# Kernel tuning notes

Hardware: AMD Instinct MI355X
Metric: run time of the kernel (lower is better)

The kernel has to match this reference:

```python
import jax, jax.numpy as jnp
import numpy as np

N = 50000      # nodes per graph batch (per siamese side)
E = 500000     # edges per side
F_IN = 128     # input_channels
H = 128        # hidden_channels
OUT = 2        # output_channels
G = 512        # number of graphs in the batch


def setup_inputs() -> dict:
    key = jax.random.key(0)
    ks = jax.random.split(key, 16)

    def lin_w(k, fan_in, shape):
        lim = 1.0 / np.sqrt(fan_in)
        return jax.random.uniform(k, shape, jnp.float32, -lim, lim)

    return {
        "x1": jax.random.normal(ks[0], (N, F_IN), jnp.float32),
        "x2": jax.random.normal(ks[1], (N, F_IN), jnp.float32),
        "edge_index1": jax.random.randint(ks[2], (2, E), 0, N, jnp.int32),
        "edge_index2": jax.random.randint(ks[3], (2, E), 0, N, jnp.int32),
        "batch1": jnp.sort(jax.random.randint(ks[4], (N,), 0, G, jnp.int32)),
        "batch2": jnp.sort(jax.random.randint(ks[5], (N,), 0, G, jnp.int32)),
        "W1": lin_w(ks[6], F_IN, (F_IN, H)), "b1": jnp.zeros((H,), jnp.float32),
        "W2": lin_w(ks[7], H, (H, H)),       "b2": jnp.zeros((H,), jnp.float32),
        "W3": lin_w(ks[8], H, (H, H)),       "b3": jnp.zeros((H,), jnp.float32),
        "Wc1": lin_w(ks[9], 2 * H, (2 * H, 4 * H)), "bc1": jnp.zeros((4 * H,), jnp.float32),
        "Wc2": lin_w(ks[10], 4 * H, (4 * H, 2 * H)), "bc2": jnp.zeros((2 * H,), jnp.float32),
        "Wc3": lin_w(ks[11], 2 * H, (2 * H, OUT)),   "bc3": jnp.zeros((OUT,), jnp.float32),
        "num_graphs": G,
    }


def _gcn_layer(x, W, b, src, dst, dinv):
    # PyG GCNConv: linear transform, then deg^{-1/2} A_hat deg^{-1/2} aggregation + bias
    h = x @ W
    msg = h[src] * (dinv[src] * dinv[dst])[:, None]   # [E+N, H]
    return jax.ops.segment_sum(msg, dst, num_segments=x.shape[0]) + b


def _forward_once(x, edge_index, batch, W1, b1, W2, b2, W3, b3, num_graphs):
    n = x.shape[0]
    loop = jnp.arange(n, dtype=edge_index.dtype)
    src = jnp.concatenate([edge_index[0], loop])      # add self-loops
    dst = jnp.concatenate([edge_index[1], loop])
    deg = jax.ops.segment_sum(jnp.ones_like(dst, dtype=x.dtype), dst, num_segments=n)
    dinv = jax.lax.rsqrt(deg)                          # deg >= 1 due to self-loops
    h = jax.nn.relu(_gcn_layer(x, W1, b1, src, dst, dinv))
    h = jax.nn.relu(_gcn_layer(h, W2, b2, src, dst, dinv))
    h = _gcn_layer(h, W3, b3, src, dst, dinv)
    # global_mean_pool over batch indices
    s = jax.ops.segment_sum(h, batch, num_segments=num_graphs)
    cnt = jax.ops.segment_sum(jnp.ones((n,), x.dtype), batch, num_segments=num_graphs)
    return s / jnp.maximum(cnt, 1.0)[:, None]


def reference(x1, x2, edge_index1, edge_index2, batch1, batch2,
              W1, b1, W2, b2, W3, b3, Wc1, bc1, Wc2, bc2, Wc3, bc3, num_graphs):
    g1 = _forward_once(x1, edge_index1, batch1, W1, b1, W2, b2, W3, b3, num_graphs)
    g2 = _forward_once(x2, edge_index2, batch2, W1, b1, W2, b2, W3, b3, num_graphs)
    z = jnp.concatenate([g1, g2], axis=1)             # [G, 2H]
    z = jax.nn.relu(z @ Wc1 + bc1)
    z = jax.nn.relu(z @ Wc2 + bc2)
    # dropout p=0.5 is identity at eval time
    return z @ Wc3 + bc3                               # [G, OUT]
```

## Files before the change

kernel.cpp:

```cpp
#include <hip/hip_runtime.h>
#include <math.h>

#define N_NODES 50000
#define E_EDGES 500000
#define HDIM    128
#define OUTC    2
#define NGRAPH  512

typedef _Float16 f16x8 __attribute__((ext_vector_type(8)));
typedef float    f32x4 __attribute__((ext_vector_type(4)));

__device__ inline float2 unpack2(unsigned u) {
    union { unsigned v; _Float16 h[2]; } c; c.v = u;
    return make_float2((float)c.h[0], (float)c.h[1]);
}
__device__ inline unsigned pack2(float a, float b) {
    union { _Float16 h[2]; unsigned u; } c;
    c.h[0] = (_Float16)a; c.h[1] = (_Float16)b;
    return c.u;
}

__global__ void k_hist(const int* __restrict__ d0, const int* __restrict__ d1,
                       int ecnt, int off1, int* __restrict__ cnt,
                       const float* __restrict__ W1, const float* __restrict__ W2,
                       _Float16* __restrict__ w1hi, _Float16* __restrict__ w1lo,
                       _Float16* __restrict__ w2hi, _Float16* __restrict__ w2lo) {
    int i = blockIdx.x * blockDim.x + threadIdx.x;
    int stride = gridDim.x * blockDim.x;
    for (int j = i; j < 128 * 128; j += stride) {
        int n = j >> 7, k = j & 127;
        float v = W1[k * 128 + n];
        _Float16 h = (_Float16)v;
        w1hi[j] = h; w1lo[j] = (_Float16)(v - (float)h);
        v = W2[k * 128 + n];
        h = (_Float16)v;
        w2hi[j] = h; w2lo[j] = (_Float16)(v - (float)h);
    }
    for (int j = i; j < ecnt; j += stride) {
        int d = (j < E_EDGES) ? d0[j] : d1[j - E_EDGES] + off1;
        atomicAdd(&cnt[d], 1);
    }
}

__global__ void k_scan_a(const int* __restrict__ cnt, int* __restrict__ excl,
                         int* __restrict__ blksum, float* __restrict__ dinv,
                         const int* __restrict__ bt0, const int* __restrict__ bt1,
                         int goff0, int nn, int nside, float* __restrict__ cnt_g) {
    __shared__ int s[512];
    int t = threadIdx.x;
    int i = blockIdx.x * 512 + t;
    int v = 0;
    if (i < nn) {
        v = cnt[i];
        dinv[i] = 1.0f / sqrtf((float)(v + 1));
        int g = (i < nside) ? bt0[i] + goff0 : bt1[i - nside] + NGRAPH;
        atomicAdd(&cnt_g[g], 1.0f);
    }
    s[t] = v; __syncthreads();
    for (int off = 1; off < 512; off <<= 1) {
        int add = (t >= off) ? s[t - off] : 0;
        __syncthreads();
        s[t] += add;
        __syncthreads();
    }
    if (i < nn) excl[i] = s[t] - v;
    if (t == 511) blksum[blockIdx.x] = s[511];
}

__global__ void k_scan_b(int* __restrict__ blksum, int nb) {
    __shared__ int s[512];
    int t = threadIdx.x;
    int v = (t < nb) ? blksum[t] : 0;
    s[t] = v; __syncthreads();
    for (int off = 1; off < 512; off <<= 1) {
        int add = (t >= off) ? s[t - off] : 0;
        __syncthreads();
        s[t] += add;
        __syncthreads();
    }
    if (t < nb) blksum[t] = s[t] - v;
}

__global__ void k_scan_c(int* __restrict__ excl, const int* __restrict__ blksum,
                         int* __restrict__ cursor, int nn, int tot) {
    int t = threadIdx.x;
    int i = blockIdx.x * 512 + t;
    if (i < nn) {
        int v = excl[i] + blksum[blockIdx.x];
        excl[i] = v;
        cursor[i] = v;
    }
    if (i == 0) excl[nn] = tot;
}

__global__ void k_fill(const int* __restrict__ s0, const int* __restrict__ s1,
                       const int* __restrict__ d0, const int* __restrict__ d1,
                       int ecnt, int off1, int goff0,
                       const int* __restrict__ bt0, const int* __restrict__ bt1,
                       int* __restrict__ cursor,
                       const float* __restrict__ dinv, int2* __restrict__ edges,
                       int* __restrict__ gdst) {
    int i = blockIdx.x * blockDim.x + threadIdx.x;
    int stride = gridDim.x * blockDim.x;
    for (; i < ecnt; i += stride) {
        int d, sg, g;
        if (i < E_EDGES) {
            int dl = d0[i];
            sg = s0[i]; d = dl; g = bt0[dl] + goff0;
        } else {
            int dl = d1[i - E_EDGES];
            sg = s1[i - E_EDGES] + off1; d = dl + off1; g = bt1[dl] + NGRAPH;
        }
        int p = atomicAdd(&cursor[d], 1);
        float w = dinv[sg] * dinv[d];
        edges[p] = make_int2(sg, __float_as_int(w));
        gdst[p] = g;
    }
}

__device__ inline void cvt8(const float4& p, const float4& q, f16x8& h, f16x8& l) {
    float v[8] = {p.x, p.y, p.z, p.w, q.x, q.y, q.z, q.w};
#pragma unroll
    for (int i = 0; i < 8; i++) {
        _Float16 hh = (_Float16)v[i];
        h[i] = hh;
        l[i] = (_Float16)(v[i] - (float)hh);
    }
}

template <int ASRC>
__global__ __launch_bounds__(256) void k_gemm_split(
        const float* __restrict__ A0f, const float* __restrict__ A1f, int nside,
        const _Float16* __restrict__ Ahi, const _Float16* __restrict__ Alo,
        const _Float16* __restrict__ Bhi, const _Float16* __restrict__ Blo,
        _Float16* __restrict__ C, int M) {
    __shared__ _Float16 sA[2][128][40];
    __shared__ _Float16 sB[2][128][40];
    int tid = threadIdx.x;
    int wave = tid >> 6, lane = tid & 63;
    int wm = (wave >> 1) * 64;
    int wn = (wave & 1) * 64;
    int quad = lane >> 4, fm = lane & 15;
    int row0 = blockIdx.x * 128;

    int lr = tid >> 2;
    int lk = (tid & 3) * 8;

    f32x4 acc[4][4] = {};
    const float4 z4 = make_float4(0.f, 0.f, 0.f, 0.f);

    for (int kc = 0; kc < 128; kc += 32) {
        int r1 = row0 + lr, r2 = row0 + lr + 64;
        bool ok1 = r1 < M, ok2 = r2 < M;
        f16x8 ah1, al1, ah2, al2;
        if (ASRC == 1) {
            const float* p1 = (r1 < nside) ? A0f + (size_t)r1 * 128
                                           : A1f + (size_t)(r1 - nside) * 128;
            const float* p2 = (r2 < nside) ? A0f + (size_t)r2 * 128
                                           : A1f + (size_t)(r2 - nside) * 128;
            float4 a = ok1 ? *(const float4*)(p1 + kc + lk) : z4;
            float4 b = ok1 ? *(const float4*)(p1 + kc + lk + 4) : z4;
            float4 c = ok2 ? *(const float4*)(p2 + kc + lk) : z4;
            float4 d = ok2 ? *(const float4*)(p2 + kc + lk + 4) : z4;
            cvt8(a, b, ah1, al1);
            cvt8(c, d, ah2, al2);
        } else {
            const f16x8 zf = {};
            ah1 = ok1 ? *(const f16x8*)(Ahi + (size_t)r1 * 128 + kc + lk) : zf;
            al1 = ok1 ? *(const f16x8*)(Alo + (size_t)r1 * 128 + kc + lk) : zf;
            ah2 = ok2 ? *(const f16x8*)(Ahi + (size_t)r2 * 128 + kc + lk) : zf;
            al2 = ok2 ? *(const f16x8*)(Alo + (size_t)r2 * 128 + kc + lk) : zf;
        }
        f16x8 bh1 = *(const f16x8*)(Bhi + (size_t)lr * 128 + kc + lk);
        f16x8 bl1 = *(const f16x8*)(Blo + (size_t)lr * 128 + kc + lk);
        f16x8 bh2 = *(const f16x8*)(Bhi + (size_t)(lr + 64) * 128 + kc + lk);
        f16x8 bl2 = *(const f16x8*)(Blo + (size_t)(lr + 64) * 128 + kc + lk);
        __syncthreads();
        *(f16x8*)&sA[0][lr][lk]      = ah1;
        *(f16x8*)&sA[1][lr][lk]      = al1;
        *(f16x8*)&sA[0][lr + 64][lk] = ah2;
        *(f16x8*)&sA[1][lr + 64][lk] = al2;
        *(f16x8*)&sB[0][lr][lk]      = bh1;
        *(f16x8*)&sB[1][lr][lk]      = bl1;
        *(f16x8*)&sB[0][lr + 64][lk] = bh2;
        *(f16x8*)&sB[1][lr + 64][lk] = bl2;
        __syncthreads();

        f16x8 afh[4], afl[4], bfh[4], bfl[4];
#pragma unroll
        for (int mi = 0; mi < 4; mi++) {
            afh[mi] = *(const f16x8*)&sA[0][wm + mi * 16 + fm][quad * 8];
            afl[mi] = *(const f16x8*)&sA[1][wm + mi * 16 + fm][quad * 8];
        }
#pragma unroll
        for (int ni = 0; ni < 4; ni++) {
            bfh[ni] = *(const f16x8*)&sB[0][wn + ni * 16 + fm][quad * 8];
            bfl[ni] = *(const f16x8*)&sB[1][wn + ni * 16 + fm][quad * 8];
        }
#pragma unroll
        for (int mi = 0; mi < 4; mi++)
#pragma unroll
            for (int ni = 0; ni < 4; ni++) {
                acc[mi][ni] = __builtin_amdgcn_mfma_f32_16x16x32_f16(afh[mi], bfh[ni], acc[mi][ni], 0, 0, 0);
                acc[mi][ni] = __builtin_amdgcn_mfma_f32_16x16x32_f16(afh[mi], bfl[ni], acc[mi][ni], 0, 0, 0);
                acc[mi][ni] = __builtin_amdgcn_mfma_f32_16x16x32_f16(afl[mi], bfh[ni], acc[mi][ni], 0, 0, 0);
            }
    }

#pragma unroll
    for (int mi = 0; mi < 4; mi++)
#pragma unroll
        for (int reg = 0; reg < 4; reg++) {
            int r = row0 + wm + mi * 16 + quad * 4 + reg;
            if (r >= M) continue;
#pragma unroll
            for (int ni = 0; ni < 4; ni++)
                C[(size_t)r * 128 + wn + ni * 16 + fm] = (_Float16)acc[mi][ni][reg];
        }
}

__global__ __launch_bounds__(256) void k_gemm(
        const float* __restrict__ A, const float* __restrict__ B,
        const float* __restrict__ bias, float* __restrict__ C,
        int M, int Nn, int K, int ldc, int act) {
    __shared__ float As[16][64];
    __shared__ float Bs[16][68];
    int tid = threadIdx.x;
    int tx = tid & 15, ty = tid >> 4;
    int row0 = blockIdx.x * 64, col0 = blockIdx.y * 64;
    float acc[4][4] = {};
    int arow = tid >> 2;
    int acol = (tid & 3) * 4;
    int brow = tid >> 4;
    int bcol = (tid & 15) * 4;

    for (int k0 = 0; k0 < K; k0 += 16) {
        float4 av = make_float4(0.f, 0.f, 0.f, 0.f);
        int ar = row0 + arow;
        if (ar < M) av = *(const float4*)(A + (size_t)ar * K + k0 + acol);
        As[acol + 0][arow] = av.x;
        As[acol + 1][arow] = av.y;
        As[acol + 2][arow] = av.z;
        As[acol + 3][arow] = av.w;

        float4 bv = make_float4(0.f, 0.f, 0.f, 0.f);
        const float* Brow = B + (size_t)(k0 + brow) * Nn;
        int bc = col0 + bcol;
        if (bc + 3 < Nn) {
            bv = *(const float4*)(Brow + bc);
        } else {
            if (bc     < Nn) bv.x = Brow[bc];
            if (bc + 1 < Nn) bv.y = Brow[bc + 1];
            if (bc + 2 < Nn) bv.z = Brow[bc + 2];
        }
        Bs[brow][bcol + 0] = bv.x;
        Bs[brow][bcol + 1] = bv.y;
        Bs[brow][bcol + 2] = bv.z;
        Bs[brow][bcol + 3] = bv.w;
        __syncthreads();

#pragma unroll
        for (int k = 0; k < 16; k++) {
            float4 a = *(const float4*)&As[k][ty * 4];
            float4 b = *(const float4*)&Bs[k][tx * 4];
            acc[0][0] += a.x * b.x; acc[0][1] += a.x * b.y; acc[0][2] += a.x * b.z; acc[0][3] += a.x * b.w;
            acc[1][0] += a.y * b.x; acc[1][1] += a.y * b.y; acc[1][2] += a.y * b.z; acc[1][3] += a.y * b.w;
            acc[2][0] += a.z * b.x; acc[2][1] += a.z * b.y; acc[2][2] += a.z * b.z; acc[2][3] += a.z * b.w;
            acc[3][0] += a.w * b.x; acc[3][1] += a.w * b.y; acc[3][2] += a.w * b.z; acc[3][3] += a.w * b.w;
        }
        __syncthreads();
    }

#pragma unroll
    for (int i = 0; i < 4; i++) {
        int r = row0 + ty * 4 + i;
        if (r >= M) continue;
#pragma unroll
        for (int j = 0; j < 4; j++) {
            int c = col0 + tx * 4 + j;
            if (c >= Nn) continue;
            float v = acc[i][j];
            if (bias) v += bias[c];
            if (act) v = fmaxf(v, 0.0f);
            C[(size_t)r * ldc + c] = v;
        }
    }
}

__global__ __launch_bounds__(256) void k_gemm_pool(
        const float* __restrict__ pool, const float* __restrict__ cnt_g,
        const float* __restrict__ W, const float* __restrict__ bias,
        float* __restrict__ zcat) {
    __shared__ float As[16][64];
    __shared__ float Bs[16][68];
    int side = blockIdx.z;
    const float* A = pool + (size_t)side * NGRAPH * HDIM;
    const float* cg = cnt_g + side * NGRAPH;
    int tid = threadIdx.x;
    int tx = tid & 15, ty = tid >> 4;
    int row0 = blockIdx.x * 64, col0 = blockIdx.y * 64;
    float acc[4][4] = {};
    int arow = tid >> 2;
    int acol = (tid & 3) * 4;
    int brow = tid >> 4;
    int bcol = (tid & 15) * 4;

    for (int k0 = 0; k0 < 128; k0 += 16) {
        int ar = row0 + arow;
        float sc = 1.0f / fmaxf(cg[ar], 1.0f);
        float4 av = *(const float4*)(A + (size_t)ar * 128 + k0 + acol);
        As[acol + 0][arow] = av.x * sc;
        As[acol + 1][arow] = av.y * sc;
        As[acol + 2][arow] = av.z * sc;
        As[acol + 3][arow] = av.w * sc;

        float4 bv = *(const float4*)(W + (size_t)(k0 + brow) * 128 + col0 + bcol);
        Bs[brow][bcol + 0] = bv.x;
        Bs[brow][bcol + 1] = bv.y;
        Bs[brow][bcol + 2] = bv.z;
        Bs[brow][bcol + 3] = bv.w;
        __syncthreads();

#pragma unroll
        for (int k = 0; k < 16; k++) {
            float4 a = *(const float4*)&As[k][ty * 4];
            float4 b = *(const float4*)&Bs[k][tx * 4];
            acc[0][0] += a.x * b.x; acc[0][1] += a.x * b.y; acc[0][2] += a.x * b.z; acc[0][3] += a.x * b.w;
            acc[1][0] += a.y * b.x; acc[1][1] += a.y * b.y; acc[1][2] += a.y * b.z; acc[1][3] += a.y * b.w;
            acc[2][0] += a.z * b.x; acc[2][1] += a.z * b.y; acc[2][2] += a.z * b.z; acc[2][3] += a.z * b.w;
            acc[3][0] += a.w * b.x; acc[3][1] += a.w * b.y; acc[3][2] += a.w * b.z; acc[3][3] += a.w * b.w;
        }
        __syncthreads();
    }

#pragma unroll
    for (int i = 0; i < 4; i++) {
        int r = row0 + ty * 4 + i;
#pragma unroll
        for (int j = 0; j < 4; j++) {
            int c = col0 + tx * 4 + j;
            zcat[(size_t)r * 256 + side * 128 + c] = acc[i][j] + bias[c];
        }
    }
}

template <int PACK>
__global__ __launch_bounds__(256) void k_agg(
        const _Float16* __restrict__ H, const float* __restrict__ dinv,
        const int* __restrict__ row_ptr, const int2* __restrict__ edges,
        const float* __restrict__ bias,
        _Float16* __restrict__ outHi, _Float16* __restrict__ outLo,
        int nnodes) {
    int wave = threadIdx.x >> 6, lane = threadIdx.x & 63;
    int node = blockIdx.x * 4 + wave;
    if (node >= nnodes) return;

    float di = dinv[node];
    float2 hv = unpack2(((const unsigned*)(H + (size_t)node * HDIM))[lane]);
    float wself = di * di;
    float ax = hv.x * wself;
    float ay = hv.y * wself;

    int rs = __builtin_amdgcn_readfirstlane(row_ptr[node]);
    int re = __builtin_amdgcn_readfirstlane(row_ptr[node + 1]);

    for (int base = rs; base < re; base += 8) {
        int nrem = re - base, m = nrem - 1;
        int i1 = 1 < nrem ? 1 : m;
        int i2 = 2 < nrem ? 2 : m;
        int i3 = 3 < nrem ? 3 : m;
        int i4 = 4 < nrem ? 4 : m;
        int i5 = 5 < nrem ? 5 : m;
        int i6 = 6 < nrem ? 6 : m;
        int i7 = 7 < nrem ? 7 : m;
        int2 E0 = edges[base];
        int2 E1 = edges[base + i1];
        int2 E2 = edges[base + i2];
        int2 E3 = edges[base + i3];
        int2 E4 = edges[base + i4];
        int2 E5 = edges[base + i5];
        int2 E6 = edges[base + i6];
        int2 E7 = edges[base + i7];
        unsigned u0 = ((const unsigned*)(H + (size_t)E0.x * HDIM))[lane];
        unsigned u1 = ((const unsigned*)(H + (size_t)E1.x * HDIM))[lane];
        unsigned u2 = ((const unsigned*)(H + (size_t)E2.x * HDIM))[lane];
        unsigned u3 = ((const unsigned*)(H + (size_t)E3.x * HDIM))[lane];
        unsigned u4 = ((const unsigned*)(H + (size_t)E4.x * HDIM))[lane];
        unsigned u5 = ((const unsigned*)(H + (size_t)E5.x * HDIM))[lane];
        unsigned u6 = ((const unsigned*)(H + (size_t)E6.x * HDIM))[lane];
        unsigned u7 = ((const unsigned*)(H + (size_t)E7.x * HDIM))[lane];
        float w0 = __int_as_float(E0.y);
        float w1 = 1 < nrem ? __int_as_float(E1.y) : 0.f;
        float w2 = 2 < nrem ? __int_as_float(E2.y) : 0.f;
        float w3 = 3 < nrem ? __int_as_float(E3.y) : 0.f;
        float w4 = 4 < nrem ? __int_as_float(E4.y) : 0.f;
        float w5 = 5 < nrem ? __int_as_float(E5.y) : 0.f;
        float w6 = 6 < nrem ? __int_as_float(E6.y) : 0.f;
        float w7 = 7 < nrem ? __int_as_float(E7.y) : 0.f;
        float2 v0 = unpack2(u0), v1 = unpack2(u1), v2 = unpack2(u2), v3 = unpack2(u3);
        float2 v4 = unpack2(u4), v5 = unpack2(u5), v6 = unpack2(u6), v7 = unpack2(u7);
        ax = fmaf(v0.x, w0, ax); ay = fmaf(v0.y, w0, ay);
        ax = fmaf(v1.x, w1, ax); ay = fmaf(v1.y, w1, ay);
        ax = fmaf(v2.x, w2, ax); ay = fmaf(v2.y, w2, ay);
        ax = fmaf(v3.x, w3, ax); ay = fmaf(v3.y, w3, ay);
        ax = fmaf(v4.x, w4, ax); ay = fmaf(v4.y, w4, ay);
        ax = fmaf(v5.x, w5, ax); ay = fmaf(v5.y, w5, ay);
        ax = fmaf(v6.x, w6, ax); ay = fmaf(v6.y, w6, ay);
        ax = fmaf(v7.x, w7, ax); ay = fmaf(v7.y, w7, ay);
    }

    float ox = fmaxf(ax + bias[lane * 2],     0.0f);
    float oy = fmaxf(ay + bias[lane * 2 + 1], 0.0f);
    if (PACK) {
        _Float16 hx = (_Float16)ox, hy = (_Float16)oy;
        _Float16 lx = (_Float16)(ox - (float)hx), ly = (_Float16)(oy - (float)hy);
        union { _Float16 h[2]; unsigned u; } ph, pl;
        ph.h[0] = hx; ph.h[1] = hy;
        pl.h[0] = lx; pl.h[1] = ly;
        ((unsigned*)(outHi + (size_t)node * HDIM))[lane] = ph.u;
        ((unsigned*)(outLo + (size_t)node * HDIM))[lane] = pl.u;
    } else {
        ((unsigned*)(outHi + (size_t)node * HDIM))[lane] = pack2(ox, oy);
    }
}

__global__ __launch_bounds__(256) void k_sweep3(
        const _Float16* __restrict__ H, const int2* __restrict__ edges,
        const int* __restrict__ gdst, const float* __restrict__ dinv,
        const int* __restrict__ bt0, const int* __restrict__ bt1,
        int goff0, int nnodes, int nside, int nedges,
        float* __restrict__ pool) {
    int lane = threadIdx.x & 63;
    int wid = blockIdx.x * 4 + (threadIdx.x >> 6);
    int ewaves = (nedges + 63) >> 6;

    if (wid < ewaves) {
        int e0 = wid << 6;
        int e1 = e0 + 64; if (e1 > nedges) e1 = nedges;
        int gfirst = __builtin_amdgcn_readfirstlane(gdst[e0]);
        int glast  = __builtin_amdgcn_readfirstlane(gdst[e1 - 1]);
        float ax = 0.f, ay = 0.f;

        if (gfirst == glast) {
            for (int base = e0; base < e1; base += 8) {
                int nrem = e1 - base, m = nrem - 1;
                int i1 = 1 < nrem ? 1 : m;
                int i2 = 2 < nrem ? 2 : m;
                int i3 = 3 < nrem ? 3 : m;
                int i4 = 4 < nrem ? 4 : m;
                int i5 = 5 < nrem ? 5 : m;
                int i6 = 6 < nrem ? 6 : m;
                int i7 = 7 < nrem ? 7 : m;
                int2 E0 = edges[base];
                int2 E1 = edges[base + i1];
                int2 E2 = edges[base + i2];
                int2 E3 = edges[base + i3];
                int2 E4 = edges[base + i4];
                int2 E5 = edges[base + i5];
                int2 E6 = edges[base + i6];
                int2 E7 = edges[base + i7];
                unsigned u0 = ((const unsigned*)(H + (size_t)E0.x * HDIM))[lane];
                unsigned u1 = ((const unsigned*)(H + (size_t)E1.x * HDIM))[lane];
                unsigned u2 = ((const unsigned*)(H + (size_t)E2.x * HDIM))[lane];
                unsigned u3 = ((const unsigned*)(H + (size_t)E3.x * HDIM))[lane];
                unsigned u4 = ((const unsigned*)(H + (size_t)E4.x * HDIM))[lane];
                unsigned u5 = ((const unsigned*)(H + (size_t)E5.x * HDIM))[lane];
                unsigned u6 = ((const unsigned*)(H + (size_t)E6.x * HDIM))[lane];
                unsigned u7 = ((const unsigned*)(H + (size_t)E7.x * HDIM))[lane];
                float w0 = __int_as_float(E0.y);
                float w1 = 1 < nrem ? __int_as_float(E1.y) : 0.f;
                float w2 = 2 < nrem ? __int_as_float(E2.y) : 0.f;
                float w3 = 3 < nrem ? __int_as_float(E3.y) : 0.f;
                float w4 = 4 < nrem ? __int_as_float(E4.y) : 0.f;
                float w5 = 5 < nrem ? __int_as_float(E5.y) : 0.f;
                float w6 = 6 < nrem ? __int_as_float(E6.y) : 0.f;
                float w7 = 7 < nrem ? __int_as_float(E7.y) : 0.f;
                float2 v0 = unpack2(u0), v1 = unpack2(u1), v2 = unpack2(u2), v3 = unpack2(u3);
                float2 v4 = unpack2(u4), v5 = unpack2(u5), v6 = unpack2(u6), v7 = unpack2(u7);
                ax = fmaf(v0.x, w0, ax); ay = fmaf(v0.y, w0, ay);
                ax = fmaf(v1.x, w1, ax); ay = fmaf(v1.y, w1, ay);
                ax = fmaf(v2.x, w2, ax); ay = fmaf(v2.y, w2, ay);
                ax = fmaf(v3.x, w3, ax); ay = fmaf(v3.y, w3, ay);
                ax = fmaf(v4.x, w4, ax); ay = fmaf(v4.y, w4, ay);
                ax = fmaf(v5.x, w5, ax); ay = fmaf(v5.y, w5, ay);
                ax = fmaf(v6.x, w6, ax); ay = fmaf(v6.y, w6, ay);
                ax = fmaf(v7.x, w7, ax); ay = fmaf(v7.y, w7, ay);
            }
            float* p = pool + (size_t)gfirst * HDIM + lane * 2;
            atomicAdd(p, ax); atomicAdd(p + 1, ay);
        } else {
            int gcur = gfirst;
            for (int e = e0; e < e1; e++) {
                int2 E = edges[e];
                int g = __builtin_amdgcn_readfirstlane(gdst[e]);
                if (g != gcur) {
                    float* p = pool + (size_t)gcur * HDIM + lane * 2;
                    atomicAdd(p, ax); atomicAdd(p + 1, ay);
                    ax = 0.f; ay = 0.f;
                    gcur = g;
                }
                float w = __int_as_float(E.y);
                float2 v = unpack2(((const unsigned*)(H + (size_t)E.x * HDIM))[lane]);
                ax = fmaf(v.x, w, ax);
                ay = fmaf(v.y, w, ay);
            }
            float* p = pool + (size_t)gcur * HDIM + lane * 2;
            atomicAdd(p, ax); atomicAdd(p + 1, ay);
        }
    } else {
        int wid2 = wid - ewaves;
        int n0 = wid2 << 6;
        if (n0 >= nnodes) return;
        int n1 = n0 + 64; if (n1 > nnodes) n1 = nnodes;
        float ax = 0.f, ay = 0.f;
        int gcur = (n0 < nside) ? bt0[n0] + goff0 : bt1[n0 - nside] + NGRAPH;
        gcur = __builtin_amdgcn_readfirstlane(gcur);
        for (int n = n0; n < n1; n++) {
            int g = (n < nside) ? bt0[n] + goff0 : bt1[n - nside] + NGRAPH;
            g = __builtin_amdgcn_readfirstlane(g);
            float dn = dinv[n];
            float w = dn * dn;
            float2 v = unpack2(((const unsigned*)(H + (size_t)n * HDIM))[lane]);
            if (g != gcur) {
                float* p = pool + (size_t)gcur * HDIM + lane * 2;
                atomicAdd(p, ax); atomicAdd(p + 1, ay);
                ax = 0.f; ay = 0.f;
                gcur = g;
            }
            ax = fmaf(v.x, w, ax);
            ay = fmaf(v.y, w, ay);
        }
        float* p = pool + (size_t)gcur * HDIM + lane * 2;
        atomicAdd(p, ax); atomicAdd(p + 1, ay);
    }
}

extern "C" void kernel_launch(void* const* d_in, const int* in_sizes, int n_in,
                              void* d_out, int out_size, void* d_ws, size_t ws_size,
                              hipStream_t stream) {
    (void)in_sizes; (void)n_in; (void)out_size;

    const float* x[2]  = {(const float*)d_in[0], (const float*)d_in[1]};
    const int*   ei[2] = {(const int*)d_in[2], (const int*)d_in[3]};
    const int*   bt[2] = {(const int*)d_in[4], (const int*)d_in[5]};
    const float* W1  = (const float*)d_in[6];  const float* b1  = (const float*)d_in[7];
    const float* W2  = (const float*)d_in[8];  const float* b2  = (const float*)d_in[9];
    const float* W3  = (const float*)d_in[10]; const float* b3  = (const float*)d_in[11];
    const float* Wc1 = (const float*)d_in[12]; const float* bc1 = (const float*)d_in[13];
    const float* Wc2 = (const float*)d_in[14]; const float* bc2 = (const float*)d_in[15];
    const float* Wc3 = (const float*)d_in[16]; const float* bc3 = (const float*)d_in[17];
    float* out = (float*)d_out;

    const bool batched = ws_size >= 120ull * 1000 * 1000;
    const int NN = batched ? 2 * N_NODES : N_NODES;
    const int NE = batched ? 2 * E_EDGES : E_EDGES;

    char* ws = (char*)d_ws;
    size_t off = 0;
    auto carve = [&](size_t bytes) -> char* {
        char* p = ws + off;
        off += (bytes + 255) & ~(size_t)255;
        return p;
    };

    int*   edge_cnt = (int*)  carve((size_t)NN * 4);
    int*   cursor   = (int*)  carve((size_t)NN * 4);
    float* pool_s   = (float*)carve((size_t)2 * NGRAPH * HDIM * 4);
    float* cnt_g    = (float*)carve((size_t)2 * NGRAPH * 4);
    float* dinv     = (float*)carve((size_t)NN * 4);
    int*   row_ptr  = (int*)  carve((size_t)(NN + 1) * 4);
    int2*  edges    = (int2*) carve((size_t)NE * 8);
    int*   gdst     = (int*)  carve((size_t)NE * 4);
    int*   blksum   = (int*)  carve(1024 * 4);
    _Float16* wt    = (_Float16*)carve(4 * 128 * 128 * 2);
    _Float16* hS    = (_Float16*)carve((size_t)NN * HDIM * 4);
    _Float16* hA    = (_Float16*)carve((size_t)NN * HDIM * 2);
    float* zcat     = (float*)carve((size_t)NGRAPH * 2 * HDIM * 4);
    float* z1       = (float*)carve((size_t)NGRAPH * 4 * HDIM * 4);
    float* z2       = (float*)carve((size_t)NGRAPH * 2 * HDIM * 4);

    _Float16* w1hi = wt;
    _Float16* w1lo = wt + 128 * 128;
    _Float16* w2hi = wt + 2 * 128 * 128;
    _Float16* w2lo = wt + 3 * 128 * 128;
    _Float16* hShi = hS;
    _Float16* hSlo = hS + (size_t)NN * HDIM;

    const int gblk = (NN + 127) / 128;
    size_t zero_all = (size_t)((char*)cnt_g + 2 * NGRAPH * 4 - (char*)edge_cnt);
    size_t zero_cnt = (size_t)((char*)pool_s - (char*)edge_cnt);

    if (batched) {
        const int nscan = (2 * N_NODES + 511) / 512;
        const int ablk  = (2 * N_NODES + 3) / 4;
        const int swaves = ((2 * E_EDGES + 63) >> 6) + ((2 * N_NODES + 63) >> 6);
        const int sblk = (swaves + 3) / 4;

        hipMemsetAsync(edge_cnt, 0, zero_all, stream);
        k_hist<<<1024, 256, 0, stream>>>(ei[0] + E_EDGES, ei[1] + E_EDGES,
                                         2 * E_EDGES, N_NODES, edge_cnt,
                                         W1, W2, w1hi, w1lo, w2hi, w2lo);
        k_scan_a<<<nscan, 512, 0, stream>>>(edge_cnt, row_ptr, blksum, dinv,
                                            bt[0], bt[1], 0, 2 * N_NODES, N_NODES, cnt_g);
        k_scan_b<<<1, 512, 0, stream>>>(blksum, nscan);
        k_scan_c<<<nscan, 512, 0, stream>>>(row_ptr, blksum, cursor, 2 * N_NODES, 2 * E_EDGES);
        k_fill<<<1024, 256, 0, stream>>>(ei[0], ei[1], ei[0] + E_EDGES, ei[1] + E_EDGES,
                                         2 * E_EDGES, N_NODES, 0, bt[0], bt[1],
                                         cursor, dinv, edges, gdst);

        k_gemm_split<1><<<gblk, 256, 0, stream>>>(x[0], x[1], N_NODES,
                                                  nullptr, nullptr, w1hi, w1lo, hA, 2 * N_NODES);
        k_agg<1><<<ablk, 256, 0, stream>>>(hA, dinv, row_ptr, edges, b1,
                                           hShi, hSlo, 2 * N_NODES);
        k_gemm_split<0><<<gblk, 256, 0, stream>>>(nullptr, nullptr, 0,
                                                  hShi, hSlo, w2hi, w2lo, hA, 2 * N_NODES);
        k_agg<0><<<ablk, 256, 0, stream>>>(hA, dinv, row_ptr, edges, b2,
                                           hShi, nullptr, 2 * N_NODES);
        k_sweep3<<<sblk, 256, 0, stream>>>(hShi, edges, gdst, dinv, bt[0], bt[1],
                                           0, 2 * N_NODES, N_NODES, 2 * E_EDGES, pool_s);
    } else {
        const int nscan = (N_NODES + 511) / 512;
        const int ablk  = (N_NODES + 3) / 4;
        const int swaves = ((E_EDGES + 63) >> 6) + ((N_NODES + 63) >> 6);
        const int sblk = (swaves + 3) / 4;

        for (int s = 0; s < 2; ++s) {
            const int* esrc = ei[s];
            const int* edst = ei[s] + E_EDGES;
            int goff = s * NGRAPH;

            hipMemsetAsync(edge_cnt, 0, s == 0 ? zero_all : zero_cnt, stream);
            k_hist<<<512, 256, 0, stream>>>(edst, edst, E_EDGES, 0, edge_cnt,
                                            W1, W2, w1hi, w1lo, w2hi, w2lo);
            k_scan_a<<<nscan, 512, 0, stream>>>(edge_cnt, row_ptr, blksum, dinv,
                                                bt[s], bt[s], goff, N_NODES, N_NODES, cnt_g);
            k_scan_b<<<1, 512, 0, stream>>>(blksum, nscan);
            k_scan_c<<<nscan, 512, 0, stream>>>(row_ptr, blksum, cursor, N_NODES, E_EDGES);
            k_fill<<<512, 256, 0, stream>>>(esrc, esrc, edst, edst, E_EDGES, 0, goff,
                                            bt[s], bt[s], cursor, dinv, edges, gdst);

            k_gemm_split<1><<<gblk, 256, 0, stream>>>(x[s], x[s], N_NODES,
                                                      nullptr, nullptr, w1hi, w1lo, hA, N_NODES);
            k_agg<1><<<ablk, 256, 0, stream>>>(hA, dinv, row_ptr, edges, b1,
                                               hShi, hSlo, N_NODES);
            k_gemm_split<0><<<gblk, 256, 0, stream>>>(nullptr, nullptr, 0,
                                                      hShi, hSlo, w2hi, w2lo, hA, N_NODES);
            k_agg<0><<<ablk, 256, 0, stream>>>(hA, dinv, row_ptr, edges, b2,
                                               hShi, nullptr, N_NODES);
            k_sweep3<<<sblk, 256, 0, stream>>>(hShi, edges, gdst, dinv, bt[s], bt[s],
                                               goff, N_NODES, N_NODES, E_EDGES, pool_s);
        }
    }

    k_gemm_pool<<<dim3(NGRAPH / 64, 2, 2), 256, 0, stream>>>(pool_s, cnt_g, W3, b3, zcat);

    k_gemm<<<dim3(NGRAPH / 64, (4 * HDIM) / 64), 256, 0, stream>>>(zcat, Wc1, bc1, z1, NGRAPH, 4 * HDIM, 2 * HDIM, 4 * HDIM, 1);
    k_gemm<<<dim3(NGRAPH / 64, (2 * HDIM) / 64), 256, 0, stream>>>(z1, Wc2, bc2, z2, NGRAPH, 2 * HDIM, 4 * HDIM, 2 * HDIM, 1);
    k_gemm<<<dim3(NGRAPH / 64, 1), 256, 0, stream>>>(z2, Wc3, bc3, out, NGRAPH, OUTC, 2 * HDIM, OUTC, 0);
}
```

Before: 589.2 us.

## Pack graph id into int4 edge records and split aggregation loops into full and tail

Each CSR edge record becomes an int4 holding source, weight and graph id, and the separate gdst array is removed. This saves one scattered store in fill and lets the pooling sweep read the graph id from the record it already loads. The aggregation kernel now runs a clamp-free full-8 loop followed by a separate masked tail, and the sweep's single-graph path is unrolled to 16 gathers per iteration to keep more loads in flight. The cost is that each edge record grows from 8 to 16 bytes with 4 padding bytes, so k_agg and the sweep read more edge-array bytes.

After: 579.4 us. Within noise of the previous version (-1.7%).

```diff
diff --git a/kernel.cpp b/kernel.cpp
--- a/kernel.cpp
+++ b/kernel.cpp
@@ -98,8 +98,7 @@
                        int ecnt, int off1, int goff0,
                        const int* __restrict__ bt0, const int* __restrict__ bt1,
                        int* __restrict__ cursor,
-                       const float* __restrict__ dinv, int2* __restrict__ edges,
-                       int* __restrict__ gdst) {
+                       const float* __restrict__ dinv, int4* __restrict__ edges) {
     int i = blockIdx.x * blockDim.x + threadIdx.x;
     int stride = gridDim.x * blockDim.x;
     for (; i < ecnt; i += stride) {
@@ -113,8 +112,7 @@
         }
         int p = atomicAdd(&cursor[d], 1);
         float w = dinv[sg] * dinv[d];
-        edges[p] = make_int2(sg, __float_as_int(w));
-        gdst[p] = g;
+        edges[p] = make_int4(sg, __float_as_int(w), g, 0);
     }
 }
 
@@ -347,7 +345,7 @@
 template <int PACK>
 __global__ __launch_bounds__(256) void k_agg(
         const _Float16* __restrict__ H, const float* __restrict__ dinv,
-        const int* __restrict__ row_ptr, const int2* __restrict__ edges,
+        const int* __restrict__ row_ptr, const int4* __restrict__ edges,
         const float* __restrict__ bias,
         _Float16* __restrict__ outHi, _Float16* __restrict__ outLo,
         int nnodes) {
@@ -364,23 +362,16 @@
     int rs = __builtin_amdgcn_readfirstlane(row_ptr[node]);
     int re = __builtin_amdgcn_readfirstlane(row_ptr[node + 1]);
 
-    for (int base = rs; base < re; base += 8) {
-        int nrem = re - base, m = nrem - 1;
-        int i1 = 1 < nrem ? 1 : m;
-        int i2 = 2 < nrem ? 2 : m;
-        int i3 = 3 < nrem ? 3 : m;
-        int i4 = 4 < nrem ? 4 : m;
-        int i5 = 5 < nrem ? 5 : m;
-        int i6 = 6 < nrem ? 6 : m;
-        int i7 = 7 < nrem ? 7 : m;
-        int2 E0 = edges[base];
-        int2 E1 = edges[base + i1];
-        int2 E2 = edges[base + i2];
-        int2 E3 = edges[base + i3];
-        int2 E4 = edges[base + i4];
-        int2 E5 = edges[base + i5];
-        int2 E6 = edges[base + i6];
-        int2 E7 = edges[base + i7];
+    int base = rs;
+    for (; base + 8 <= re; base += 8) {
+        int4 E0 = edges[base + 0];
+        int4 E1 = edges[base + 1];
+        int4 E2 = edges[base + 2];
+        int4 E3 = edges[base + 3];
+        int4 E4 = edges[base + 4];
+        int4 E5 = edges[base + 5];
+        int4 E6 = edges[base + 6];
+        int4 E7 = edges[base + 7];
         unsigned u0 = ((const unsigned*)(H + (size_t)E0.x * HDIM))[lane];
         unsigned u1 = ((const unsigned*)(H + (size_t)E1.x * HDIM))[lane];
         unsigned u2 = ((const unsigned*)(H + (size_t)E2.x * HDIM))[lane];
@@ -389,16 +380,12 @@
         unsigned u5 = ((const unsigned*)(H + (size_t)E5.x * HDIM))[lane];
         unsigned u6 = ((const unsigned*)(H + (size_t)E6.x * HDIM))[lane];
         unsigned u7 = ((const unsigned*)(H + (size_t)E7.x * HDIM))[lane];
-        float w0 = __int_as_float(E0.y);
-        float w1 = 1 < nrem ? __int_as_float(E1.y) : 0.f;
-        float w2 = 2 < nrem ? __int_as_float(E2.y) : 0.f;
-        float w3 = 3 < nrem ? __int_as_float(E3.y) : 0.f;
-        float w4 = 4 < nrem ? __int_as_float(E4.y) : 0.f;
-        float w5 = 5 < nrem ? __int_as_float(E5.y) : 0.f;
-        float w6 = 6 < nrem ? __int_as_float(E6.y) : 0.f;
-        float w7 = 7 < nrem ? __int_as_float(E7.y) : 0.f;
         float2 v0 = unpack2(u0), v1 = unpack2(u1), v2 = unpack2(u2), v3 = unpack2(u3);
         float2 v4 = unpack2(u4), v5 = unpack2(u5), v6 = unpack2(u6), v7 = unpack2(u7);
+        float w0 = __int_as_float(E0.y), w1 = __int_as_float(E1.y);
+        float w2 = __int_as_float(E2.y), w3 = __int_as_float(E3.y);
+        float w4 = __int_as_float(E4.y), w5 = __int_as_float(E5.y);
+        float w6 = __int_as_float(E6.y), w7 = __int_as_float(E7.y);
         ax = fmaf(v0.x, w0, ax); ay = fmaf(v0.y, w0, ay);
         ax = fmaf(v1.x, w1, ax); ay = fmaf(v1.y, w1, ay);
         ax = fmaf(v2.x, w2, ax); ay = fmaf(v2.y, w2, ay);
@@ -407,6 +394,39 @@
         ax = fmaf(v5.x, w5, ax); ay = fmaf(v5.y, w5, ay);
         ax = fmaf(v6.x, w6, ax); ay = fmaf(v6.y, w6, ay);
         ax = fmaf(v7.x, w7, ax); ay = fmaf(v7.y, w7, ay);
+    }
+    if (base < re) {
+        int nrem = re - base, m = nrem - 1;
+        int4 E0 = edges[base];
+        int4 E1 = edges[base + (1 < nrem ? 1 : m)];
+        int4 E2 = edges[base + (2 < nrem ? 2 : m)];
+        int4 E3 = edges[base + (3 < nrem ? 3 : m)];
+        int4 E4 = edges[base + (4 < nrem ? 4 : m)];
+        int4 E5 = edges[base + (5 < nrem ? 5 : m)];
+        int4 E6 = edges[base + (6 < nrem ? 6 : m)];
+        unsigned u0 = ((const unsigned*)(H + (size_t)E0.x * HDIM))[lane];
+        unsigned u1 = ((const unsigned*)(H + (size_t)E1.x * HDIM))[lane];
+        unsigned u2 = ((const unsigned*)(H + (size_t)E2.x * HDIM))[lane];
+        unsigned u3 = ((const unsigned*)(H + (size_t)E3.x * HDIM))[lane];
+        unsigned u4 = ((const unsigned*)(H + (size_t)E4.x * HDIM))[lane];
+        unsigned u5 = ((const unsigned*)(H + (size_t)E5.x * HDIM))[lane];
+        unsigned u6 = ((const unsigned*)(H + (size_t)E6.x * HDIM))[lane];
+        float2 v0 = unpack2(u0), v1 = unpack2(u1), v2 = unpack2(u2), v3 = unpack2(u3);
+        float2 v4 = unpack2(u4), v5 = unpack2(u5), v6 = unpack2(u6);
+        float w0 = __int_as_float(E0.y);
+        float w1 = 1 < nrem ? __int_as_float(E1.y) : 0.f;
+        float w2 = 2 < nrem ? __int_as_float(E2.y) : 0.f;
+        float w3 = 3 < nrem ? __int_as_float(E3.y) : 0.f;
+        float w4 = 4 < nrem ? __int_as_float(E4.y) : 0.f;
+        float w5 = 5 < nrem ? __int_as_float(E5.y) : 0.f;
+        float w6 = 6 < nrem ? __int_as_float(E6.y) : 0.f;
+        ax = fmaf(v0.x, w0, ax); ay = fmaf(v0.y, w0, ay);
+        ax = fmaf(v1.x, w1, ax); ay = fmaf(v1.y, w1, ay);
+        ax = fmaf(v2.x, w2, ax); ay = fmaf(v2.y, w2, ay);
+        ax = fmaf(v3.x, w3, ax); ay = fmaf(v3.y, w3, ay);
+        ax = fmaf(v4.x, w4, ax); ay = fmaf(v4.y, w4, ay);
+        ax = fmaf(v5.x, w5, ax); ay = fmaf(v5.y, w5, ay);
+        ax = fmaf(v6.x, w6, ax); ay = fmaf(v6.y, w6, ay);
     }
 
     float ox = fmaxf(ax + bias[lane * 2],     0.0f);
@@ -425,8 +445,8 @@
 }
 
 __global__ __launch_bounds__(256) void k_sweep3(
-        const _Float16* __restrict__ H, const int2* __restrict__ edges,
-        const int* __restrict__ gdst, const float* __restrict__ dinv,
+        const _Float16* __restrict__ H, const int4* __restrict__ edges,
+        const float* __restrict__ dinv,
         const int* __restrict__ bt0, const int* __restrict__ bt1,
         int goff0, int nnodes, int nside, int nedges,
         float* __restrict__ pool) {
@@ -437,62 +457,61 @@
     if (wid < ewaves) {
         int e0 = wid << 6;
         int e1 = e0 + 64; if (e1 > nedges) e1 = nedges;
-        int gfirst = __builtin_amdgcn_readfirstlane(gdst[e0]);
-        int glast  = __builtin_amdgcn_readfirstlane(gdst[e1 - 1]);
+        int gfirst = __builtin_amdgcn_readfirstlane(edges[e0].z);
+        int glast  = __builtin_amdgcn_readfirstlane(edges[e1 - 1].z);
         float ax = 0.f, ay = 0.f;
 
         if (gfirst == glast) {
-            for (int base = e0; base < e1; base += 8) {
-                int nrem = e1 - base, m = nrem - 1;
-                int i1 = 1 < nrem ? 1 : m;
-                int i2 = 2 < nrem ? 2 : m;
-                int i3 = 3 < nrem ? 3 : m;
-                int i4 = 4 < nrem ? 4 : m;
-                int i5 = 5 < nrem ? 5 : m;
-                int i6 = 6 < nrem ? 6 : m;
-                int i7 = 7 < nrem ? 7 : m;
-                int2 E0 = edges[base];
-                int2 E1 = edges[base + i1];
-                int2 E2 = edges[base + i2];
-                int2 E3 = edges[base + i3];
-                int2 E4 = edges[base + i4];
-                int2 E5 = edges[base + i5];
-                int2 E6 = edges[base + i6];
-                int2 E7 = edges[base + i7];
-                unsigned u0 = ((const unsigned*)(H + (size_t)E0.x * HDIM))[lane];
-                unsigned u1 = ((const unsigned*)(H + (size_t)E1.x * HDIM))[lane];
-                unsigned u2 = ((const unsigned*)(H + (size_t)E2.x * HDIM))[lane];
-                unsigned u3 = ((const unsigned*)(H + (size_t)E3.x * HDIM))[lane];
-                unsigned u4 = ((const unsigned*)(H + (size_t)E4.x * HDIM))[lane];
-                unsigned u5 = ((const unsigned*)(H + (size_t)E5.x * HDIM))[lane];
-                unsigned u6 = ((const unsigned*)(H + (size_t)E6.x * HDIM))[lane];
-                unsigned u7 = ((const unsigned*)(H + (size_t)E7.x * HDIM))[lane];
-                float w0 = __int_as_float(E0.y);
-                float w1 = 1 < nrem ? __int_as_float(E1.y) : 0.f;
-                float w2 = 2 < nrem ? __int_as_float(E2.y) : 0.f;
-                float w3 = 3 < nrem ? __int_as_float(E3.y) : 0.f;
-                float w4 = 4 < nrem ? __int_as_float(E4.y) : 0.f;
-                float w5 = 5 < nrem ? __int_as_float(E5.y) : 0.f;
-                float w6 = 6 < nrem ? __int_as_float(E6.y) : 0.f;
-                float w7 = 7 < nrem ? __int_as_float(E7.y) : 0.f;
-                float2 v0 = unpack2(u0), v1 = unpack2(u1), v2 = unpack2(u2), v3 = unpack2(u3);
-                float2 v4 = unpack2(u4), v5 = unpack2(u5), v6 = unpack2(u6), v7 = unpack2(u7);
-                ax = fmaf(v0.x, w0, ax); ay = fmaf(v0.y, w0, ay);
-                ax = fmaf(v1.x, w1, ax); ay = fmaf(v1.y, w1, ay);
-                ax = fmaf(v2.x, w2, ax); ay = fmaf(v2.y, w2, ay);
-                ax = fmaf(v3.x, w3, ax); ay = fmaf(v3.y, w3, ay);
-                ax = fmaf(v4.x, w4, ax); ay = fmaf(v4.y, w4, ay);
-                ax = fmaf(v5.x, w5, ax); ay = fmaf(v5.y, w5, ay);
-                ax = fmaf(v6.x, w6, ax); ay = fmaf(v6.y, w6, ay);
-                ax = fmaf(v7.x, w7, ax); ay = fmaf(v7.y, w7, ay);
+            int base = e0;
+            for (; base + 16 <= e1; base += 16) {
+                unsigned u[16];
+                float w[16];
+#pragma unroll
+                for (int j = 0; j < 16; j += 4) {
+                    int4 Ea = edges[base + j + 0];
+                    int4 Eb = edges[base + j + 1];
+                    int4 Ec = edges[base + j + 2];
+                    int4 Ed = edges[base + j + 3];
+                    u[j + 0] = ((const unsigned*)(H + (size_t)Ea.x * HDIM))[lane];
+                    u[j + 1] = ((const unsigned*)(H + (size_t)Eb.x * HDIM))[lane];
+                    u[j + 2] = ((const unsigned*)(H + (size_t)Ec.x * HDIM))[lane];
+                    u[j + 3] = ((const unsigned*)(H + (size_t)Ed.x * HDIM))[lane];
+                    w[j + 0] = __int_as_float(Ea.y);
+                    w[j + 1] = __int_as_float(Eb.y);
+                    w[j + 2] = __int_as_float(Ec.y);
+                    w[j + 3] = __int_as_float(Ed.y);
+                }
+#pragma unroll
+                for (int j = 0; j < 16; j++) {
+                    float2 v = unpack2(u[j]);
+                    ax = fmaf(v.x, w[j], ax);
+                    ay = fmaf(v.y, w[j], ay);
+                }
+            }
+            for (; base + 8 <= e1; base += 8) {
+#pragma unroll
+                for (int j = 0; j < 8; j++) {
+                    int4 E = edges[base + j];
+                    float2 v = unpack2(((const unsigned*)(H + (size_t)E.x * HDIM))[lane]);
+                    float wj = __int_as_float(E.y);
+                    ax = fmaf(v.x, wj, ax);
+                    ay = fmaf(v.y, wj, ay);
+                }
+            }
+            for (; base < e1; base++) {
+                int4 E = edges[base];
+                float2 v = unpack2(((const unsigned*)(H + (size_t)E.x * HDIM))[lane]);
+                float wj = __int_as_float(E.y);
+                ax = fmaf(v.x, wj, ax);
+                ay = fmaf(v.y, wj, ay);
             }
             float* p = pool + (size_t)gfirst * HDIM + lane * 2;
             atomicAdd(p, ax); atomicAdd(p + 1, ay);
         } else {
             int gcur = gfirst;
             for (int e = e0; e < e1; e++) {
-                int2 E = edges[e];
-                int g = __builtin_amdgcn_readfirstlane(gdst[e]);
+                int4 E = edges[e];
+                int g = __builtin_amdgcn_readfirstlane(E.z);
                 if (g != gcur) {
                     float* p = pool + (size_t)gcur * HDIM + lane * 2;
                     atomicAdd(p, ax); atomicAdd(p + 1, ay);
@@ -569,8 +588,7 @@
     float* cnt_g    = (float*)carve((size_t)2 * NGRAPH * 4);
     float* dinv     = (float*)carve((size_t)NN * 4);
     int*   row_ptr  = (int*)  carve((size_t)(NN + 1) * 4);
-    int2*  edges    = (int2*) carve((size_t)NE * 8);
-    int*   gdst     = (int*)  carve((size_t)NE * 4);
+    int4*  edges    = (int4*) carve((size_t)NE * 16);
     int*   blksum   = (int*)  carve(1024 * 4);
     _Float16* wt    = (_Float16*)carve(4 * 128 * 128 * 2);
     _Float16* hS    = (_Float16*)carve((size_t)NN * HDIM * 4);
@@ -606,7 +624,7 @@
         k_scan_c<<<nscan, 512, 0, stream>>>(row_ptr, blksum, cursor, 2 * N_NODES, 2 * E_EDGES);
         k_fill<<<1024, 256, 0, stream>>>(ei[0], ei[1], ei[0] + E_EDGES, ei[1] + E_EDGES,
                                          2 * E_EDGES, N_NODES, 0, bt[0], bt[1],
-                                         cursor, dinv, edges, gdst);
+                                         cursor, dinv, edges);
 
         k_gemm_split<1><<<gblk, 256, 0, stream>>>(x[0], x[1], N_NODES,
                                                   nullptr, nullptr, w1hi, w1lo, hA, 2 * N_NODES);
@@ -616,7 +634,7 @@
                                                   hShi, hSlo, w2hi, w2lo, hA, 2 * N_NODES);
         k_agg<0><<<ablk, 256, 0, stream>>>(hA, dinv, row_ptr, edges, b2,
                                            hShi, nullptr, 2 * N_NODES);
-        k_sweep3<<<sblk, 256, 0, stream>>>(hShi, edges, gdst, dinv, bt[0], bt[1],
+        k_sweep3<<<sblk, 256, 0, stream>>>(hShi, edges, dinv, bt[0], bt[1],
                                            0, 2 * N_NODES, N_NODES, 2 * E_EDGES, pool_s);
     } else {
         const int nscan = (N_NODES + 511) / 512;
@@ -637,7 +655,7 @@
             k_scan_b<<<1, 512, 0, stream>>>(blksum, nscan);
             k_scan_c<<<nscan, 512, 0, stream>>>(row_ptr, blksum, cursor, N_NODES, E_EDGES);
             k_fill<<<512, 256, 0, stream>>>(esrc, esrc, edst, edst, E_EDGES, 0, goff,
-                                            bt[s], bt[s], cursor, dinv, edges, gdst);
+                                            bt[s], bt[s], cursor, dinv, edges);
 
             k_gemm_split<1><<<gblk, 256, 0, stream>>>(x[s], x[s], N_NODES,
                                                       nullptr, nullptr, w1hi, w1lo, hA, N_NODES);
@@ -647,7 +665,7 @@
                                                       hShi, hSlo, w2hi, w2lo, hA, N_NODES);
             k_agg<0><<<ablk, 256, 0, stream>>>(hA, dinv, row_ptr, edges, b2,
                                                hShi, nullptr, N_NODES);
-            k_sweep3<<<sblk, 256, 0, stream>>>(hShi, edges, gdst, dinv, bt[s], bt[s],
+            k_sweep3<<<sblk, 256, 0, stream>>>(hShi, edges, dinv, bt[s], bt[s],
                                                goff, N_NODES, N_NODES, E_EDGES, pool_s);
         }
     }
```
